# Kernel tuning notes

Measured on AMD Instinct MI355X. Metric: run time of the kernel, lower is better.

## Reference

```python
import jax, jax.numpy as jnp
import numpy as np

D = 256
N_EDGES = 8192
N_CORNERS = 4096


def setup_inputs() -> dict:
    key = jax.random.key(0)
    ks = jax.random.split(key, 8)
    scale = 1.0 / np.sqrt(D)
    return {
        "edge_pred": jax.random.uniform(ks[0], (N_EDGES,), dtype=jnp.float32),
        "edge_corner": jax.random.randint(ks[1], (N_EDGES, 2), 0, N_CORNERS, dtype=jnp.int64),
        "all_corners": jax.random.uniform(ks[2], (N_CORNERS, 2), dtype=jnp.float32),
        "edge_x": jax.random.normal(ks[3], (N_EDGES, D), dtype=jnp.float32),
        "image_x": jax.random.normal(ks[4], (1024,), dtype=jnp.float32),
        "W1": jax.random.normal(ks[5], (D, D), dtype=jnp.float32) * scale,
        "b1": jnp.zeros((D,), dtype=jnp.float32),
        "W2": jax.random.normal(ks[6], (D, D), dtype=jnp.float32) * scale,
        "b2": jnp.zeros((D,), dtype=jnp.float32),
        "W3": jax.random.normal(ks[7], (3 * D, D), dtype=jnp.float32) * scale,
        "b3": jnp.zeros((D,), dtype=jnp.float32),
    }


def _linear_block(x, W, b):
    # LinearBlock: Linear followed by ReLU
    return jax.nn.relu(x @ W + b)


def reference(edge_pred, edge_corner, all_corners, edge_x, image_x, W1, b1, W2, b2, W3, b3):
    # 'fully' branch of MPModule.forward. edge_pred/edge_corner/all_corners/image_x
    # are unused in this branch (kept for signature fidelity).
    e1 = _linear_block(edge_x, W1, b1)              # [N, D]
    # (e1.unsqueeze(1) * e1).mean(-1) == (e1 @ e1.T) / D   -> [N, N]
    sim1 = (e1 @ e1.T) / D
    e2 = _linear_block(edge_x, W2, b2)
    sim2 = (e2 @ e2.T) / D
    # (edge_x * sim.unsqueeze(-1)).sum(1) == sim @ edge_x  -> [N, D]
    agg1 = sim1 @ edge_x
    agg2 = sim2 @ edge_x
    cat = jnp.concatenate([edge_x, agg1, agg2], axis=-1)  # [N, 3D]
    out = _linear_block(cat, W3, b3)                      # [N, D]
    return out
```

## Files before the change

### kernel.cpp

```cpp
#include <hip/hip_runtime.h>

#define NE 8192
#define DD 256
#define NSPLIT 16

typedef __attribute__((ext_vector_type(8))) short short8;
typedef __attribute__((ext_vector_type(4))) short short4v;
typedef __attribute__((ext_vector_type(8))) __bf16 bf16x8;
typedef __attribute__((ext_vector_type(4))) float floatx4;

__device__ __forceinline__ unsigned short f2bf(float f) {
  union { float f; unsigned int i; } v; v.f = f;
  unsigned int r = v.i + 0x7fffu + ((v.i >> 16) & 1u);
  return (unsigned short)(r >> 16);
}

__device__ __forceinline__ floatx4 mfma_bf16(short8 a, short8 b, floatx4 c) {
  return __builtin_amdgcn_mfma_f32_16x16x32_bf16(
      __builtin_bit_cast(bf16x8, a), __builtin_bit_cast(bf16x8, b), c, 0, 0, 0);
}

__device__ __forceinline__ void tcvt_tile(float* ls,
                                          const float* __restrict__ src, int C,
                                          unsigned short* __restrict__ dst, int R,
                                          int r0, int c0, int tid) {
  const int rr = tid >> 4, c4 = (tid & 15) * 4;
#pragma unroll
  for (int k = 0; k < 4; ++k)
    *(floatx4*)&ls[(rr + k * 16) * 68 + c4] =
        *(const floatx4*)&src[(size_t)(r0 + rr + k * 16) * C + c0 + c4];
  __syncthreads();
  const int cc = tid >> 2, rb = (tid & 3) * 16;
  short8 o0, o1;
#pragma unroll
  for (int i = 0; i < 8; ++i) {
    o0[i] = (short)f2bf(ls[(rb + i) * 68 + cc]);
    o1[i] = (short)f2bf(ls[(rb + 8 + i) * 68 + cc]);
  }
  unsigned short* dp = &dst[(size_t)(c0 + cc) * R + r0 + rb];
  *(short8*)dp = o0;
  *(short8*)(dp + 8) = o1;
}

__global__ void cvt_all(const float* __restrict__ x, unsigned short* __restrict__ xb,
                        unsigned short* __restrict__ xT,
                        const float* __restrict__ W1, unsigned short* __restrict__ W1t,
                        const float* __restrict__ W2, unsigned short* __restrict__ W2t,
                        const float* __restrict__ W3, unsigned short* __restrict__ W3t0) {
  __shared__ float ls[64 * 68];
  const int b = blockIdx.x, tid = threadIdx.x;
  if (b < 512) {
    const int p = b & 7, k = b >> 3;
    const int r0 = (16 * p + (k >> 2)) * 64, c0 = (k & 3) * 64;
    const int rr = tid >> 4, c4 = (tid & 15) * 4;
#pragma unroll
    for (int kk = 0; kk < 4; ++kk) {
      floatx4 v = *(const floatx4*)&x[(size_t)(r0 + rr + kk * 16) * DD + c0 + c4];
      *(floatx4*)&ls[(rr + kk * 16) * 68 + c4] = v;
      short4v s;
#pragma unroll
      for (int c = 0; c < 4; ++c) s[c] = (short)f2bf(v[c]);
      *(short4v*)&xb[(size_t)(r0 + rr + kk * 16) * DD + c0 + c4] = s;
    }
    __syncthreads();
    const int cc = tid >> 2, rb = (tid & 3) * 16;
    short8 o0, o1;
#pragma unroll
    for (int i = 0; i < 8; ++i) {
      o0[i] = (short)f2bf(ls[(rb + i) * 68 + cc]);
      o1[i] = (short)f2bf(ls[(rb + 8 + i) * 68 + cc]);
    }
    unsigned short* dp = &xT[(size_t)(c0 + cc) * NE + r0 + rb];
    *(short8*)dp = o0;
    *(short8*)(dp + 8) = o1;
  } else {
    int t = b - 512;
    const float* src = (t < 16) ? W1 : ((t < 32) ? W2 : W3);
    unsigned short* dst = (t < 16) ? W1t : ((t < 32) ? W2t : W3t0);
    t &= 15;
    tcvt_tile(ls, src, DD, dst, DD, (t >> 2) * 64, (t & 3) * 64, tid);
  }
}

__global__ __launch_bounds__(256, 3)
void e_gemm(const unsigned short* __restrict__ xb,
            const unsigned short* __restrict__ W1t, const float* __restrict__ b1,
            const unsigned short* __restrict__ W2t, const float* __restrict__ b2,
            unsigned short* __restrict__ e1, unsigned short* __restrict__ e2,
            unsigned short* __restrict__ e1T, unsigned short* __restrict__ e2T)
{
  __shared__ __align__(16) unsigned short smA[64 * 136];
  __shared__ __align__(16) unsigned short smB1[64 * 136];
  __shared__ __align__(16) unsigned short smB2[64 * 136];
  const int T = threadIdx.x, lane = T & 63, wv = T >> 6;
  const int q = lane >> 4, r = lane & 15;
  const int L = blockIdx.x;
  const int p = L & 7, k = L >> 3;
  const int col0 = (k & 3) * 64, row0 = (16 * p + (k >> 2)) * 64;

  floatx4 acc1[4], acc2[4];
#pragma unroll
  for (int j = 0; j < 4; ++j) {
    acc1[j] = (floatx4){0.f, 0.f, 0.f, 0.f};
    acc2[j] = (floatx4){0.f, 0.f, 0.f, 0.f};
  }

  short8 pa[4], pb1[4], pb2[4];
#pragma unroll
  for (int pp = 0; pp < 4; ++pp) {
    const int id = pp * 256 + T, rr = id >> 4, k8 = (id & 15) * 8;
    pa[pp]  = *(const short8*)&xb[(size_t)(row0 + rr) * DD + k8];
    pb1[pp] = *(const short8*)&W1t[(size_t)(col0 + rr) * DD + k8];
    pb2[pp] = *(const short8*)&W2t[(size_t)(col0 + rr) * DD + k8];
  }

  for (int kc = 0; kc < 256; kc += 128) {
#pragma unroll
    for (int pp = 0; pp < 4; ++pp) {
      const int id = pp * 256 + T, rr = id >> 4, k8 = (id & 15) * 8;
      *(short8*)&smA[rr * 136 + k8]  = pa[pp];
      *(short8*)&smB1[rr * 136 + k8] = pb1[pp];
      *(short8*)&smB2[rr * 136 + k8] = pb2[pp];
    }
    __syncthreads();
    if (kc + 128 < 256) {
#pragma unroll
      for (int pp = 0; pp < 4; ++pp) {
        const int id = pp * 256 + T, rr = id >> 4, k8 = (id & 15) * 8;
        pa[pp]  = *(const short8*)&xb[(size_t)(row0 + rr) * DD + kc + 128 + k8];
        pb1[pp] = *(const short8*)&W1t[(size_t)(col0 + rr) * DD + kc + 128 + k8];
        pb2[pp] = *(const short8*)&W2t[(size_t)(col0 + rr) * DD + kc + 128 + k8];
      }
    }
#pragma unroll
    for (int ks = 0; ks < 4; ++ks) {
      short8 af = *(const short8*)&smA[(wv * 16 + r) * 136 + ks * 32 + q * 8];
#pragma unroll
      for (int j = 0; j < 4; ++j) {
        short8 b1f = *(const short8*)&smB1[(j * 16 + r) * 136 + ks * 32 + q * 8];
        short8 b2f = *(const short8*)&smB2[(j * 16 + r) * 136 + ks * 32 + q * 8];
        acc1[j] = mfma_bf16(af, b1f, acc1[j]);
        acc2[j] = mfma_bf16(af, b2f, acc2[j]);
      }
    }
    __syncthreads();
  }

  unsigned short* t1s = smB1;
  unsigned short* t2s = smB2;
#pragma unroll
  for (int j = 0; j < 4; ++j) {
    const int col = col0 + j * 16 + r;
    const int lc = j * 16 + r;
    const int lr = wv * 16 + q * 4;
    const int rowb = row0 + lr;
    const float b1v = b1[col], b2v = b2[col];
#pragma unroll
    for (int t = 0; t < 4; ++t) {
      unsigned short h1 = f2bf(fmaxf(acc1[j][t] + b1v, 0.0f));
      unsigned short h2 = f2bf(fmaxf(acc2[j][t] + b2v, 0.0f));
      t1s[lc * 68 + lr + t] = h1;
      t2s[lc * 68 + lr + t] = h2;
      e1[(size_t)(rowb + t) * DD + col] = h1;
      e2[(size_t)(rowb + t) * DD + col] = h2;
    }
  }
  __syncthreads();
  {
    const int c = T >> 2, seg = (T & 3) * 16;
    short8 v1a = *(short8*)&t1s[c * 68 + seg];
    short8 v1b = *(short8*)&t1s[c * 68 + seg + 8];
    short8 v2a = *(short8*)&t2s[c * 68 + seg];
    short8 v2b = *(short8*)&t2s[c * 68 + seg + 8];
    unsigned short* d1 = &e1T[(size_t)(col0 + c) * NE + row0 + seg];
    unsigned short* d2 = &e2T[(size_t)(col0 + c) * NE + row0 + seg];
    *(short8*)d1 = v1a; *(short8*)(d1 + 8) = v1b;
    *(short8*)d2 = v2a; *(short8*)(d2 + 8) = v2b;
  }
}

__global__ __launch_bounds__(256, 4)
void atb(const unsigned short* __restrict__ e1T, const unsigned short* __restrict__ e2T,
         const unsigned short* __restrict__ xT, float* __restrict__ P_T)
{
  __shared__ __align__(16) unsigned short smA[64 * 136];
  __shared__ __align__(16) unsigned short smB[64 * 136];
  const int T = threadIdx.x, lane = T & 63, wv = T >> 6;
  const int q = lane >> 4, r = lane & 15;
  const int L = blockIdx.x;
  const int p = L & 7, k = L >> 3;
  const int y = 2 * p + (k & 1);
  const int t2 = k >> 1;
  const int mn = t2 & 15, z = t2 >> 4;
  const int m0 = (mn >> 2) * 64, n0 = (mn & 3) * 64;
  const int j0 = y * (NE / NSPLIT);
  const unsigned short* E = z ? e2T : e1T;
  float* P = P_T + (size_t)(z * NSPLIT + y) * 65536;

  floatx4 acc[4];
#pragma unroll
  for (int j = 0; j < 4; ++j) acc[j] = (floatx4){0.f, 0.f, 0.f, 0.f};

  short8 pa[4], pb[4];
#pragma unroll
  for (int pp = 0; pp < 4; ++pp) {
    const int id = pp * 256 + T, mm = id >> 4, j8 = (id & 15) * 8;
    pa[pp] = *(const short8*)&E[(size_t)(m0 + mm) * NE + j0 + j8];
    pb[pp] = *(const short8*)&xT[(size_t)(n0 + mm) * NE + j0 + j8];
  }

  for (int jc = 0; jc < NE / NSPLIT; jc += 128) {
#pragma unroll
    for (int pp = 0; pp < 4; ++pp) {
      const int id = pp * 256 + T, mm = id >> 4, j8 = (id & 15) * 8;
      *(short8*)&smA[mm * 136 + j8] = pa[pp];
      *(short8*)&smB[mm * 136 + j8] = pb[pp];
    }
    __syncthreads();
    if (jc + 128 < NE / NSPLIT) {
#pragma unroll
      for (int pp = 0; pp < 4; ++pp) {
        const int id = pp * 256 + T, mm = id >> 4, j8 = (id & 15) * 8;
        pa[pp] = *(const short8*)&E[(size_t)(m0 + mm) * NE + j0 + jc + 128 + j8];
        pb[pp] = *(const short8*)&xT[(size_t)(n0 + mm) * NE + j0 + jc + 128 + j8];
      }
    }
#pragma unroll
    for (int ks = 0; ks < 4; ++ks) {
      short8 af = *(const short8*)&smA[(wv * 16 + r) * 136 + ks * 32 + q * 8];
#pragma unroll
      for (int j = 0; j < 4; ++j) {
        short8 bf = *(const short8*)&smB[(j * 16 + r) * 136 + ks * 32 + q * 8];
        acc[j] = mfma_bf16(af, bf, acc[j]);
      }
    }
    __syncthreads();
  }
#pragma unroll
  for (int j = 0; j < 4; ++j) {
    const int n = n0 + j * 16 + r;
    const int m = m0 + wv * 16 + q * 4;
    *(floatx4*)&P[(size_t)n * DD + m] = acc[j];
  }
}

__global__ void reduce_g(const float* __restrict__ P_T, float* __restrict__ G_T) {
  int idx = blockIdx.x * 256 + threadIdx.x;
  int z = idx >> 14, off = idx & 16383;
  const floatx4* Pp = (const floatx4*)P_T;
  floatx4 s = (floatx4){0.f, 0.f, 0.f, 0.f};
#pragma unroll
  for (int y = 0; y < NSPLIT; ++y)
    s += Pp[(size_t)(z * NSPLIT + y) * 16384 + off];
  ((floatx4*)G_T)[idx] = s;
}

__global__ __launch_bounds__(256, 2)
void h_mfma(const float* __restrict__ G_T, const float* __restrict__ W3,
            unsigned short* __restrict__ H1t, unsigned short* __restrict__ H2t)
{
  __shared__ __align__(16) unsigned short smA[64 * 136];
  __shared__ __align__(16) unsigned short smB[64 * 136];
  const int T = threadIdx.x, lane = T & 63, wv = T >> 6;
  const int q = lane >> 4, r = lane & 15;
  const int z = blockIdx.z;
  const int me0 = (blockIdx.x >> 2) * 64, m30 = (blockIdx.x & 3) * 64;
  const float* G = G_T + (size_t)z * 65536;
  unsigned short* Ht = z ? H2t : H1t;
  const int woff = 256 + z * 256;

  floatx4 acc[4];
#pragma unroll
  for (int j = 0; j < 4; ++j) acc[j] = (floatx4){0.f, 0.f, 0.f, 0.f};

  for (int lc = 0; lc < 256; lc += 128) {
#pragma unroll
    for (int pp = 0; pp < 2; ++pp) {
      const int id = pp * 256 + T, lb = id >> 4, e4 = id & 15;
      floatx4 grow[4], wrow[4];
#pragma unroll
      for (int i = 0; i < 4; ++i) {
        grow[i] = *(const floatx4*)&G[(size_t)(lc + lb * 4 + i) * DD + me0 + e4 * 4];
        wrow[i] = *(const floatx4*)&W3[(size_t)(woff + lc + lb * 4 + i) * DD + m30 + e4 * 4];
      }
#pragma unroll
      for (int s4 = 0; s4 < 4; ++s4) {
        const int c = (s4 + e4) & 3;
        short4v ga = {(short)f2bf(grow[0][c] * 0.00390625f),
                      (short)f2bf(grow[1][c] * 0.00390625f),
                      (short)f2bf(grow[2][c] * 0.00390625f),
                      (short)f2bf(grow[3][c] * 0.00390625f)};
        short4v wa = {(short)f2bf(wrow[0][c]), (short)f2bf(wrow[1][c]),
                      (short)f2bf(wrow[2][c]), (short)f2bf(wrow[3][c])};
        *(short4v*)&smA[(e4 * 4 + c) * 136 + lb * 4] = ga;
        *(short4v*)&smB[(e4 * 4 + c) * 136 + lb * 4] = wa;
      }
    }
    __syncthreads();
#pragma unroll
    for (int ks = 0; ks < 4; ++ks) {
      short8 af = *(const short8*)&smA[(wv * 16 + r) * 136 + ks * 32 + q * 8];
#pragma unroll
      for (int j = 0; j < 4; ++j) {
        short8 bf = *(const short8*)&smB[(j * 16 + r) * 136 + ks * 32 + q * 8];
        acc[j] = mfma_bf16(af, bf, acc[j]);
      }
    }
    __syncthreads();
  }
#pragma unroll
  for (int j = 0; j < 4; ++j) {
    const int m3 = m30 + j * 16 + r;
    const int me = me0 + wv * 16 + q * 4;
    short4v v;
#pragma unroll
    for (int i = 0; i < 4; ++i) v[i] = (short)f2bf(acc[j][i]);
    *(short4v*)&Ht[(size_t)m3 * DD + me] = v;
  }
}

__global__ __launch_bounds__(256, 4)
void out_gemm(const unsigned short* __restrict__ xb,
              const unsigned short* __restrict__ e1, const unsigned short* __restrict__ e2,
              const unsigned short* __restrict__ W3t0,
              const unsigned short* __restrict__ H1t, const unsigned short* __restrict__ H2t,
              const float* __restrict__ b3, float* __restrict__ out)
{
  __shared__ __align__(16) unsigned short smA[64 * 136];
  __shared__ __align__(16) unsigned short smB[64 * 136];
  const int T = threadIdx.x, lane = T & 63, wv = T >> 6;
  const int q = lane >> 4, r = lane & 15;
  const int L = blockIdx.x;
  const int p = L & 7, k = L >> 3;
  const int col0 = (k & 3) * 64, row0 = (16 * p + (k >> 2)) * 64;

  const unsigned short* As[3] = {xb, e1, e2};
  const unsigned short* Bs[3] = {W3t0, H1t, H2t};

  floatx4 acc[4];
#pragma unroll
  for (int j = 0; j < 4; ++j) acc[j] = (floatx4){0.f, 0.f, 0.f, 0.f};

  short8 qa[4], qb[4];
#pragma unroll
  for (int pp = 0; pp < 4; ++pp) {
    const int id = pp * 256 + T, rr = id >> 4, k8 = (id & 15) * 8;
    qa[pp] = *(const short8*)&As[0][(size_t)(row0 + rr) * DD + k8];
    qb[pp] = *(const short8*)&Bs[0][(size_t)(col0 + rr) * DD + k8];
  }

  for (int rd = 0; rd < 6; ++rd) {
#pragma unroll
    for (int pp = 0; pp < 4; ++pp) {
      const int id = pp * 256 + T, rr = id >> 4, k8 = (id & 15) * 8;
      *(short8*)&smA[rr * 136 + k8] = qa[pp];
      *(short8*)&smB[rr * 136 + k8] = qb[pp];
    }
    __syncthreads();
    if (rd + 1 < 6) {
      const int s = (rd + 1) >> 1, kc = ((rd + 1) & 1) * 128;
      const unsigned short* A = As[s];
      const unsigned short* B = Bs[s];
#pragma unroll
      for (int pp = 0; pp < 4; ++pp) {
        const int id = pp * 256 + T, rr = id >> 4, k8 = (id & 15) * 8;
        qa[pp] = *(const short8*)&A[(size_t)(row0 + rr) * DD + kc + k8];
        qb[pp] = *(const short8*)&B[(size_t)(col0 + rr) * DD + kc + k8];
      }
    }
#pragma unroll
    for (int ks = 0; ks < 4; ++ks) {
      short8 af = *(const short8*)&smA[(wv * 16 + r) * 136 + ks * 32 + q * 8];
#pragma unroll
      for (int j = 0; j < 4; ++j) {
        short8 bf = *(const short8*)&smB[(j * 16 + r) * 136 + ks * 32 + q * 8];
        acc[j] = mfma_bf16(af, bf, acc[j]);
      }
    }
    __syncthreads();
  }
#pragma unroll
  for (int j = 0; j < 4; ++j) {
    const int col = col0 + j * 16 + r;
    const float bv = b3[col];
    const int rowb = row0 + wv * 16 + q * 4;
#pragma unroll
    for (int t = 0; t < 4; ++t)
      out[(size_t)(rowb + t) * DD + col] = fmaxf(acc[j][t] + bv, 0.0f);
  }
}

extern "C" void kernel_launch(void* const* d_in, const int* in_sizes, int n_in,
                              void* d_out, int out_size, void* d_ws, size_t ws_size,
                              hipStream_t stream) {
  (void)in_sizes; (void)n_in; (void)out_size; (void)ws_size;
  const float* x  = (const float*)d_in[3];
  const float* W1 = (const float*)d_in[5];
  const float* b1 = (const float*)d_in[6];
  const float* W2 = (const float*)d_in[7];
  const float* b2 = (const float*)d_in[8];
  const float* W3 = (const float*)d_in[9];
  const float* b3 = (const float*)d_in[10];
  float* out = (float*)d_out;

  char* ws = (char*)d_ws;
  const size_t MB = 1u << 20;
  const size_t KB = 1u << 10;
  unsigned short* xb   = (unsigned short*)ws;
  unsigned short* xT   = (unsigned short*)(ws + 4 * MB);
  unsigned short* e1   = (unsigned short*)(ws + 8 * MB);
  unsigned short* e2   = (unsigned short*)(ws + 12 * MB);
  unsigned short* e1T  = (unsigned short*)(ws + 16 * MB);
  unsigned short* e2T  = (unsigned short*)(ws + 20 * MB);
  unsigned short* W1t  = (unsigned short*)(ws + 24 * MB);
  unsigned short* W2t  = (unsigned short*)(ws + 24 * MB + 128 * KB);
  unsigned short* W3t0 = (unsigned short*)(ws + 24 * MB + 256 * KB);
  unsigned short* H1t  = (unsigned short*)(ws + 24 * MB + 384 * KB);
  unsigned short* H2t  = (unsigned short*)(ws + 24 * MB + 512 * KB);
  float* G_T           = (float*)(ws + 24 * MB + 640 * KB);
  float* P_T           = (float*)(ws + 25 * MB);

  cvt_all<<<560, 256, 0, stream>>>(x, xb, xT, W1, W1t, W2, W2t, W3, W3t0);
  e_gemm<<<512, 256, 0, stream>>>(xb, W1t, b1, W2t, b2, e1, e2, e1T, e2T);
  atb<<<512, 256, 0, stream>>>(e1T, e2T, xT, P_T);
  reduce_g<<<128, 256, 0, stream>>>(P_T, G_T);
  h_mfma<<<dim3(16, 1, 2), 256, 0, stream>>>(G_T, W3, H1t, H2t);
  out_gemm<<<512, 256, 0, stream>>>(xb, e1, e2, W3t0, H1t, H2t, b3, out);
}
```

Before: 120.4 us.

## Fuse all six stages into one persistent kernel with grid barriers

Replaces the six separate launches (convert, e-GEMM, A^T·B partials, reduction, H GEMM, output GEMM) with one persistent kernel of 256 blocks. Each block handles two tiles per stage, and stages are separated by an atomic-counter grid barrier. The aim is to remove inter-kernel launch gaps and tail drain between the small stages. The partial-sum buffer is aliased onto the output buffer, and a memset resets the barrier counter on every call. In exchange, each CU runs only one 4-wave block instead of several resident blocks, so there is less latency hiding. Correctness also depends on all 256 blocks being co-resident.

```diff
diff --git a/kernel.cpp b/kernel.cpp
--- a/kernel.cpp
+++ b/kernel.cpp
@@ -3,6 +3,7 @@
 #define NE 8192
 #define DD 256
 #define NSPLIT 16
+#define NBLK 256
 
 typedef __attribute__((ext_vector_type(8))) short short8;
 typedef __attribute__((ext_vector_type(4))) short short4v;
@@ -18,6 +19,18 @@
 __device__ __forceinline__ floatx4 mfma_bf16(short8 a, short8 b, floatx4 c) {
   return __builtin_amdgcn_mfma_f32_16x16x32_bf16(
       __builtin_bit_cast(bf16x8, a), __builtin_bit_cast(bf16x8, b), c, 0, 0, 0);
+}
+
+__device__ __forceinline__ void gbar(unsigned* bar, unsigned target) {
+  __syncthreads();
+  if (threadIdx.x == 0) {
+    __threadfence();
+    __hip_atomic_fetch_add(bar, 1u, __ATOMIC_ACQ_REL, __HIP_MEMORY_SCOPE_AGENT);
+    while (__hip_atomic_load(bar, __ATOMIC_ACQUIRE, __HIP_MEMORY_SCOPE_AGENT) < target)
+      __builtin_amdgcn_s_sleep(1);
+    __threadfence();
+  }
+  __syncthreads();
 }
 
 __device__ __forceinline__ void tcvt_tile(float* ls,
@@ -42,351 +55,348 @@
   *(short8*)(dp + 8) = o1;
 }
 
-__global__ void cvt_all(const float* __restrict__ x, unsigned short* __restrict__ xb,
-                        unsigned short* __restrict__ xT,
-                        const float* __restrict__ W1, unsigned short* __restrict__ W1t,
-                        const float* __restrict__ W2, unsigned short* __restrict__ W2t,
-                        const float* __restrict__ W3, unsigned short* __restrict__ W3t0) {
-  __shared__ float ls[64 * 68];
-  const int b = blockIdx.x, tid = threadIdx.x;
-  if (b < 512) {
-    const int p = b & 7, k = b >> 3;
-    const int r0 = (16 * p + (k >> 2)) * 64, c0 = (k & 3) * 64;
-    const int rr = tid >> 4, c4 = (tid & 15) * 4;
-#pragma unroll
-    for (int kk = 0; kk < 4; ++kk) {
-      floatx4 v = *(const floatx4*)&x[(size_t)(r0 + rr + kk * 16) * DD + c0 + c4];
-      *(floatx4*)&ls[(rr + kk * 16) * 68 + c4] = v;
-      short4v s;
-#pragma unroll
-      for (int c = 0; c < 4; ++c) s[c] = (short)f2bf(v[c]);
-      *(short4v*)&xb[(size_t)(r0 + rr + kk * 16) * DD + c0 + c4] = s;
-    }
-    __syncthreads();
-    const int cc = tid >> 2, rb = (tid & 3) * 16;
-    short8 o0, o1;
-#pragma unroll
-    for (int i = 0; i < 8; ++i) {
-      o0[i] = (short)f2bf(ls[(rb + i) * 68 + cc]);
-      o1[i] = (short)f2bf(ls[(rb + 8 + i) * 68 + cc]);
-    }
-    unsigned short* dp = &xT[(size_t)(c0 + cc) * NE + r0 + rb];
-    *(short8*)dp = o0;
-    *(short8*)(dp + 8) = o1;
-  } else {
-    int t = b - 512;
-    const float* src = (t < 16) ? W1 : ((t < 32) ? W2 : W3);
-    unsigned short* dst = (t < 16) ? W1t : ((t < 32) ? W2t : W3t0);
-    t &= 15;
-    tcvt_tile(ls, src, DD, dst, DD, (t >> 2) * 64, (t & 3) * 64, tid);
-  }
-}
-
-__global__ __launch_bounds__(256, 3)
-void e_gemm(const unsigned short* __restrict__ xb,
-            const unsigned short* __restrict__ W1t, const float* __restrict__ b1,
-            const unsigned short* __restrict__ W2t, const float* __restrict__ b2,
-            unsigned short* __restrict__ e1, unsigned short* __restrict__ e2,
-            unsigned short* __restrict__ e1T, unsigned short* __restrict__ e2T)
+__global__ __launch_bounds__(256, 2)
+void mega(const float* __restrict__ x,
+          const float* __restrict__ W1, const float* __restrict__ b1,
+          const float* __restrict__ W2, const float* __restrict__ b2,
+          const float* __restrict__ W3, const float* __restrict__ b3,
+          float* __restrict__ out,
+          unsigned short* __restrict__ xb, unsigned short* __restrict__ xT,
+          unsigned short* __restrict__ e1, unsigned short* __restrict__ e2,
+          unsigned short* __restrict__ e1T, unsigned short* __restrict__ e2T,
+          unsigned short* __restrict__ W1t, unsigned short* __restrict__ W2t,
+          unsigned short* __restrict__ W3t0,
+          unsigned short* __restrict__ H1t, unsigned short* __restrict__ H2t,
+          float* __restrict__ G_T, float* __restrict__ P_T,
+          unsigned* bar)
 {
-  __shared__ __align__(16) unsigned short smA[64 * 136];
-  __shared__ __align__(16) unsigned short smB1[64 * 136];
-  __shared__ __align__(16) unsigned short smB2[64 * 136];
-  const int T = threadIdx.x, lane = T & 63, wv = T >> 6;
+  __shared__ __align__(16) unsigned short smPool[3 * 64 * 136];
+  unsigned short* smA  = smPool;
+  unsigned short* smB1 = smPool + 64 * 136;
+  unsigned short* smB2 = smPool + 2 * 64 * 136;
+  const int b = blockIdx.x, T = threadIdx.x;
+  const int lane = T & 63, wv = T >> 6;
   const int q = lane >> 4, r = lane & 15;
-  const int L = blockIdx.x;
-  const int p = L & 7, k = L >> 3;
-  const int col0 = (k & 3) * 64, row0 = (16 * p + (k >> 2)) * 64;
-
-  floatx4 acc1[4], acc2[4];
-#pragma unroll
-  for (int j = 0; j < 4; ++j) {
-    acc1[j] = (floatx4){0.f, 0.f, 0.f, 0.f};
-    acc2[j] = (floatx4){0.f, 0.f, 0.f, 0.f};
-  }
-
-  short8 pa[4], pb1[4], pb2[4];
-#pragma unroll
-  for (int pp = 0; pp < 4; ++pp) {
-    const int id = pp * 256 + T, rr = id >> 4, k8 = (id & 15) * 8;
-    pa[pp]  = *(const short8*)&xb[(size_t)(row0 + rr) * DD + k8];
-    pb1[pp] = *(const short8*)&W1t[(size_t)(col0 + rr) * DD + k8];
-    pb2[pp] = *(const short8*)&W2t[(size_t)(col0 + rr) * DD + k8];
-  }
-
-  for (int kc = 0; kc < 256; kc += 128) {
+
+  {
+    float* ls = (float*)smPool;
+#pragma unroll
+    for (int h = 0; h < 2; ++h) {
+      const int L = b + h * NBLK;
+      const int p = L & 7, k = L >> 3;
+      const int r0 = (16 * p + (k >> 2)) * 64, c0 = (k & 3) * 64;
+      const int rr = T >> 4, c4 = (T & 15) * 4;
+#pragma unroll
+      for (int kk = 0; kk < 4; ++kk) {
+        floatx4 v = *(const floatx4*)&x[(size_t)(r0 + rr + kk * 16) * DD + c0 + c4];
+        *(floatx4*)&ls[(rr + kk * 16) * 68 + c4] = v;
+        short4v s;
+#pragma unroll
+        for (int c = 0; c < 4; ++c) s[c] = (short)f2bf(v[c]);
+        *(short4v*)&xb[(size_t)(r0 + rr + kk * 16) * DD + c0 + c4] = s;
+      }
+      __syncthreads();
+      const int cc = T >> 2, rb = (T & 3) * 16;
+      short8 o0, o1;
+#pragma unroll
+      for (int i = 0; i < 8; ++i) {
+        o0[i] = (short)f2bf(ls[(rb + i) * 68 + cc]);
+        o1[i] = (short)f2bf(ls[(rb + 8 + i) * 68 + cc]);
+      }
+      unsigned short* dp = &xT[(size_t)(c0 + cc) * NE + r0 + rb];
+      *(short8*)dp = o0;
+      *(short8*)(dp + 8) = o1;
+      __syncthreads();
+    }
+    if (b < 48) {
+      int t = b;
+      const float* src = (t < 16) ? W1 : ((t < 32) ? W2 : W3);
+      unsigned short* dst = (t < 16) ? W1t : ((t < 32) ? W2t : W3t0);
+      t &= 15;
+      tcvt_tile(ls, src, DD, dst, DD, (t >> 2) * 64, (t & 3) * 64, T);
+    }
+  }
+  gbar(bar, 1 * NBLK);
+
+#pragma unroll 1
+  for (int h = 0; h < 2; ++h) {
+    const int L = b + h * NBLK;
+    const int p = L & 7, k = L >> 3;
+    const int col0 = (k & 3) * 64, row0 = (16 * p + (k >> 2)) * 64;
+
+    floatx4 acc1[4], acc2[4];
+#pragma unroll
+    for (int j = 0; j < 4; ++j) {
+      acc1[j] = (floatx4){0.f, 0.f, 0.f, 0.f};
+      acc2[j] = (floatx4){0.f, 0.f, 0.f, 0.f};
+    }
+
+    short8 pa[4], pb1[4], pb2[4];
 #pragma unroll
     for (int pp = 0; pp < 4; ++pp) {
       const int id = pp * 256 + T, rr = id >> 4, k8 = (id & 15) * 8;
-      *(short8*)&smA[rr * 136 + k8]  = pa[pp];
-      *(short8*)&smB1[rr * 136 + k8] = pb1[pp];
-      *(short8*)&smB2[rr * 136 + k8] = pb2[pp];
-    }
-    __syncthreads();
-    if (kc + 128 < 256) {
+      pa[pp]  = *(const short8*)&xb[(size_t)(row0 + rr) * DD + k8];
+      pb1[pp] = *(const short8*)&W1t[(size_t)(col0 + rr) * DD + k8];
+      pb2[pp] = *(const short8*)&W2t[(size_t)(col0 + rr) * DD + k8];
+    }
+
+    for (int kc = 0; kc < 256; kc += 128) {
 #pragma unroll
       for (int pp = 0; pp < 4; ++pp) {
         const int id = pp * 256 + T, rr = id >> 4, k8 = (id & 15) * 8;
-        pa[pp]  = *(const short8*)&xb[(size_t)(row0 + rr) * DD + kc + 128 + k8];
-        pb1[pp] = *(const short8*)&W1t[(size_t)(col0 + rr) * DD + kc + 128 + k8];
-        pb2[pp] = *(const short8*)&W2t[(size_t)(col0 + rr) * DD + kc + 128 + k8];
-      }
-    }
-#pragma unroll
-    for (int ks = 0; ks < 4; ++ks) {
-      short8 af = *(const short8*)&smA[(wv * 16 + r) * 136 + ks * 32 + q * 8];
-#pragma unroll
-      for (int j = 0; j < 4; ++j) {
-        short8 b1f = *(const short8*)&smB1[(j * 16 + r) * 136 + ks * 32 + q * 8];
-        short8 b2f = *(const short8*)&smB2[(j * 16 + r) * 136 + ks * 32 + q * 8];
-        acc1[j] = mfma_bf16(af, b1f, acc1[j]);
-        acc2[j] = mfma_bf16(af, b2f, acc2[j]);
+        *(short8*)&smA[rr * 136 + k8]  = pa[pp];
+        *(short8*)&smB1[rr * 136 + k8] = pb1[pp];
+        *(short8*)&smB2[rr * 136 + k8] = pb2[pp];
+      }
+      __syncthreads();
+      if (kc + 128 < 256) {
+#pragma unroll
+        for (int pp = 0; pp < 4; ++pp) {
+          const int id = pp * 256 + T, rr = id >> 4, k8 = (id & 15) * 8;
+          pa[pp]  = *(const short8*)&xb[(size_t)(row0 + rr) * DD + kc + 128 + k8];
+          pb1[pp] = *(const short8*)&W1t[(size_t)(col0 + rr) * DD + kc + 128 + k8];
+          pb2[pp] = *(const short8*)&W2t[(size_t)(col0 + rr) * DD + kc + 128 + k8];
+        }
+      }
+#pragma unroll
+      for (int ks = 0; ks < 4; ++ks) {
+        short8 af = *(const short8*)&smA[(wv * 16 + r) * 136 + ks * 32 + q * 8];
+#pragma unroll
+        for (int j = 0; j < 4; ++j) {
+          short8 b1f = *(const short8*)&smB1[(j * 16 + r) * 136 + ks * 32 + q * 8];
+          short8 b2f = *(const short8*)&smB2[(j * 16 + r) * 136 + ks * 32 + q * 8];
+          acc1[j] = mfma_bf16(af, b1f, acc1[j]);
+          acc2[j] = mfma_bf16(af, b2f, acc2[j]);
+        }
+      }
+      __syncthreads();
+    }
+
+    unsigned short* t1s = smB1;
+    unsigned short* t2s = smB2;
+#pragma unroll
+    for (int j = 0; j < 4; ++j) {
+      const int col = col0 + j * 16 + r;
+      const int lc = j * 16 + r;
+      const int lr = wv * 16 + q * 4;
+      const int rowb = row0 + lr;
+      const float b1v = b1[col], b2v = b2[col];
+#pragma unroll
+      for (int t = 0; t < 4; ++t) {
+        unsigned short h1 = f2bf(fmaxf(acc1[j][t] + b1v, 0.0f));
+        unsigned short h2 = f2bf(fmaxf(acc2[j][t] + b2v, 0.0f));
+        t1s[lc * 68 + lr + t] = h1;
+        t2s[lc * 68 + lr + t] = h2;
+        e1[(size_t)(rowb + t) * DD + col] = h1;
+        e2[(size_t)(rowb + t) * DD + col] = h2;
       }
     }
     __syncthreads();
-  }
-
-  unsigned short* t1s = smB1;
-  unsigned short* t2s = smB2;
-#pragma unroll
-  for (int j = 0; j < 4; ++j) {
-    const int col = col0 + j * 16 + r;
-    const int lc = j * 16 + r;
-    const int lr = wv * 16 + q * 4;
-    const int rowb = row0 + lr;
-    const float b1v = b1[col], b2v = b2[col];
-#pragma unroll
-    for (int t = 0; t < 4; ++t) {
-      unsigned short h1 = f2bf(fmaxf(acc1[j][t] + b1v, 0.0f));
-      unsigned short h2 = f2bf(fmaxf(acc2[j][t] + b2v, 0.0f));
-      t1s[lc * 68 + lr + t] = h1;
-      t2s[lc * 68 + lr + t] = h2;
-      e1[(size_t)(rowb + t) * DD + col] = h1;
-      e2[(size_t)(rowb + t) * DD + col] = h2;
-    }
-  }
-  __syncthreads();
-  {
-    const int c = T >> 2, seg = (T & 3) * 16;
-    short8 v1a = *(short8*)&t1s[c * 68 + seg];
-    short8 v1b = *(short8*)&t1s[c * 68 + seg + 8];
-    short8 v2a = *(short8*)&t2s[c * 68 + seg];
-    short8 v2b = *(short8*)&t2s[c * 68 + seg + 8];
-    unsigned short* d1 = &e1T[(size_t)(col0 + c) * NE + row0 + seg];
-    unsigned short* d2 = &e2T[(size_t)(col0 + c) * NE + row0 + seg];
-    *(short8*)d1 = v1a; *(short8*)(d1 + 8) = v1b;
-    *(short8*)d2 = v2a; *(short8*)(d2 + 8) = v2b;
-  }
-}
-
-__global__ __launch_bounds__(256, 4)
-void atb(const unsigned short* __restrict__ e1T, const unsigned short* __restrict__ e2T,
-         const unsigned short* __restrict__ xT, float* __restrict__ P_T)
-{
-  __shared__ __align__(16) unsigned short smA[64 * 136];
-  __shared__ __align__(16) unsigned short smB[64 * 136];
-  const int T = threadIdx.x, lane = T & 63, wv = T >> 6;
-  const int q = lane >> 4, r = lane & 15;
-  const int L = blockIdx.x;
-  const int p = L & 7, k = L >> 3;
-  const int y = 2 * p + (k & 1);
-  const int t2 = k >> 1;
-  const int mn = t2 & 15, z = t2 >> 4;
-  const int m0 = (mn >> 2) * 64, n0 = (mn & 3) * 64;
-  const int j0 = y * (NE / NSPLIT);
-  const unsigned short* E = z ? e2T : e1T;
-  float* P = P_T + (size_t)(z * NSPLIT + y) * 65536;
-
-  floatx4 acc[4];
-#pragma unroll
-  for (int j = 0; j < 4; ++j) acc[j] = (floatx4){0.f, 0.f, 0.f, 0.f};
-
-  short8 pa[4], pb[4];
-#pragma unroll
-  for (int pp = 0; pp < 4; ++pp) {
-    const int id = pp * 256 + T, mm = id >> 4, j8 = (id & 15) * 8;
-    pa[pp] = *(const short8*)&E[(size_t)(m0 + mm) * NE + j0 + j8];
-    pb[pp] = *(const short8*)&xT[(size_t)(n0 + mm) * NE + j0 + j8];
-  }
-
-  for (int jc = 0; jc < NE / NSPLIT; jc += 128) {
+    {
+      const int c = T >> 2, seg = (T & 3) * 16;
+      short8 v1a = *(short8*)&t1s[c * 68 + seg];
+      short8 v1b = *(short8*)&t1s[c * 68 + seg + 8];
+      short8 v2a = *(short8*)&t2s[c * 68 + seg];
+      short8 v2b = *(short8*)&t2s[c * 68 + seg + 8];
+      unsigned short* d1 = &e1T[(size_t)(col0 + c) * NE + row0 + seg];
+      unsigned short* d2 = &e2T[(size_t)(col0 + c) * NE + row0 + seg];
+      *(short8*)d1 = v1a; *(short8*)(d1 + 8) = v1b;
+      *(short8*)d2 = v2a; *(short8*)(d2 + 8) = v2b;
+    }
+    __syncthreads();
+  }
+  gbar(bar, 2 * NBLK);
+
+#pragma unroll 1
+  for (int h = 0; h < 2; ++h) {
+    const int L = b + h * NBLK;
+    const int p = L & 7, k = L >> 3;
+    const int y = 2 * p + (k & 1);
+    const int t2 = k >> 1;
+    const int mn = t2 & 15, z = t2 >> 4;
+    const int m0 = (mn >> 2) * 64, n0 = (mn & 3) * 64;
+    const int j0 = y * (NE / NSPLIT);
+    const unsigned short* E = z ? e2T : e1T;
+    float* P = P_T + (size_t)(z * NSPLIT + y) * 65536;
+
+    floatx4 acc[4];
+#pragma unroll
+    for (int j = 0; j < 4; ++j) acc[j] = (floatx4){0.f, 0.f, 0.f, 0.f};
+
+    short8 pa[4], pb[4];
 #pragma unroll
     for (int pp = 0; pp < 4; ++pp) {
       const int id = pp * 256 + T, mm = id >> 4, j8 = (id & 15) * 8;
-      *(short8*)&smA[mm * 136 + j8] = pa[pp];
-      *(short8*)&smB[mm * 136 + j8] = pb[pp];
-    }
-    __syncthreads();
-    if (jc + 128 < NE / NSPLIT) {
+      pa[pp] = *(const short8*)&E[(size_t)(m0 + mm) * NE + j0 + j8];
+      pb[pp] = *(const short8*)&xT[(size_t)(n0 + mm) * NE + j0 + j8];
+    }
+
+    for (int jc = 0; jc < NE / NSPLIT; jc += 128) {
 #pragma unroll
       for (int pp = 0; pp < 4; ++pp) {
         const int id = pp * 256 + T, mm = id >> 4, j8 = (id & 15) * 8;
-        pa[pp] = *(const short8*)&E[(size_t)(m0 + mm) * NE + j0 + jc + 128 + j8];
-        pb[pp] = *(const short8*)&xT[(size_t)(n0 + mm) * NE + j0 + jc + 128 + j8];
-      }
-    }
-#pragma unroll
-    for (int ks = 0; ks < 4; ++ks) {
-      short8 af = *(const short8*)&smA[(wv * 16 + r) * 136 + ks * 32 + q * 8];
-#pragma unroll
-      for (int j = 0; j < 4; ++j) {
-        short8 bf = *(const short8*)&smB[(j * 16 + r) * 136 + ks * 32 + q * 8];
-        acc[j] = mfma_bf16(af, bf, acc[j]);
-      }
-    }
-    __syncthreads();
-  }
-#pragma unroll
-  for (int j = 0; j < 4; ++j) {
-    const int n = n0 + j * 16 + r;
-    const int m = m0 + wv * 16 + q * 4;
-    *(floatx4*)&P[(size_t)n * DD + m] = acc[j];
-  }
-}
-
-__global__ void reduce_g(const float* __restrict__ P_T, float* __restrict__ G_T) {
-  int idx = blockIdx.x * 256 + threadIdx.x;
-  int z = idx >> 14, off = idx & 16383;
-  const floatx4* Pp = (const floatx4*)P_T;
-  floatx4 s = (floatx4){0.f, 0.f, 0.f, 0.f};
-#pragma unroll
-  for (int y = 0; y < NSPLIT; ++y)
-    s += Pp[(size_t)(z * NSPLIT + y) * 16384 + off];
-  ((floatx4*)G_T)[idx] = s;
-}
-
-__global__ __launch_bounds__(256, 2)
-void h_mfma(const float* __restrict__ G_T, const float* __restrict__ W3,
-            unsigned short* __restrict__ H1t, unsigned short* __restrict__ H2t)
-{
-  __shared__ __align__(16) unsigned short smA[64 * 136];
-  __shared__ __align__(16) unsigned short smB[64 * 136];
-  const int T = threadIdx.x, lane = T & 63, wv = T >> 6;
-  const int q = lane >> 4, r = lane & 15;
-  const int z = blockIdx.z;
-  const int me0 = (blockIdx.x >> 2) * 64, m30 = (blockIdx.x & 3) * 64;
-  const float* G = G_T + (size_t)z * 65536;
-  unsigned short* Ht = z ? H2t : H1t;
-  const int woff = 256 + z * 256;
-
-  floatx4 acc[4];
-#pragma unroll
-  for (int j = 0; j < 4; ++j) acc[j] = (floatx4){0.f, 0.f, 0.f, 0.f};
-
-  for (int lc = 0; lc < 256; lc += 128) {
-#pragma unroll
-    for (int pp = 0; pp < 2; ++pp) {
-      const int id = pp * 256 + T, lb = id >> 4, e4 = id & 15;
-      floatx4 grow[4], wrow[4];
-#pragma unroll
-      for (int i = 0; i < 4; ++i) {
-        grow[i] = *(const floatx4*)&G[(size_t)(lc + lb * 4 + i) * DD + me0 + e4 * 4];
-        wrow[i] = *(const floatx4*)&W3[(size_t)(woff + lc + lb * 4 + i) * DD + m30 + e4 * 4];
-      }
-#pragma unroll
-      for (int s4 = 0; s4 < 4; ++s4) {
-        const int c = (s4 + e4) & 3;
-        short4v ga = {(short)f2bf(grow[0][c] * 0.00390625f),
-                      (short)f2bf(grow[1][c] * 0.00390625f),
-                      (short)f2bf(grow[2][c] * 0.00390625f),
-                      (short)f2bf(grow[3][c] * 0.00390625f)};
-        short4v wa = {(short)f2bf(wrow[0][c]), (short)f2bf(wrow[1][c]),
-                      (short)f2bf(wrow[2][c]), (short)f2bf(wrow[3][c])};
-        *(short4v*)&smA[(e4 * 4 + c) * 136 + lb * 4] = ga;
-        *(short4v*)&smB[(e4 * 4 + c) * 136 + lb * 4] = wa;
-      }
-    }
-    __syncthreads();
-#pragma unroll
-    for (int ks = 0; ks < 4; ++ks) {
-      short8 af = *(const short8*)&smA[(wv * 16 + r) * 136 + ks * 32 + q * 8];
-#pragma unroll
-      for (int j = 0; j < 4; ++j) {
-        short8 bf = *(const short8*)&smB[(j * 16 + r) * 136 + ks * 32 + q * 8];
-        acc[j] = mfma_bf16(af, bf, acc[j]);
-      }
-    }
-    __syncthreads();
-  }
-#pragma unroll
-  for (int j = 0; j < 4; ++j) {
-    const int m3 = m30 + j * 16 + r;
-    const int me = me0 + wv * 16 + q * 4;
-    short4v v;
-#pragma unroll
-    for (int i = 0; i < 4; ++i) v[i] = (short)f2bf(acc[j][i]);
-    *(short4v*)&Ht[(size_t)m3 * DD + me] = v;
-  }
-}
-
-__global__ __launch_bounds__(256, 4)
-void out_gemm(const unsigned short* __restrict__ xb,
-              const unsigned short* __restrict__ e1, const unsigned short* __restrict__ e2,
-              const unsigned short* __restrict__ W3t0,
-              const unsigned short* __restrict__ H1t, const unsigned short* __restrict__ H2t,
-              const float* __restrict__ b3, float* __restrict__ out)
-{
-  __shared__ __align__(16) unsigned short smA[64 * 136];
-  __shared__ __align__(16) unsigned short smB[64 * 136];
-  const int T = threadIdx.x, lane = T & 63, wv = T >> 6;
-  const int q = lane >> 4, r = lane & 15;
-  const int L = blockIdx.x;
-  const int p = L & 7, k = L >> 3;
-  const int col0 = (k & 3) * 64, row0 = (16 * p + (k >> 2)) * 64;
-
-  const unsigned short* As[3] = {xb, e1, e2};
-  const unsigned short* Bs[3] = {W3t0, H1t, H2t};
-
-  floatx4 acc[4];
-#pragma unroll
-  for (int j = 0; j < 4; ++j) acc[j] = (floatx4){0.f, 0.f, 0.f, 0.f};
-
-  short8 qa[4], qb[4];
-#pragma unroll
-  for (int pp = 0; pp < 4; ++pp) {
-    const int id = pp * 256 + T, rr = id >> 4, k8 = (id & 15) * 8;
-    qa[pp] = *(const short8*)&As[0][(size_t)(row0 + rr) * DD + k8];
-    qb[pp] = *(const short8*)&Bs[0][(size_t)(col0 + rr) * DD + k8];
-  }
-
-  for (int rd = 0; rd < 6; ++rd) {
+        *(short8*)&smA[mm * 136 + j8] = pa[pp];
+        *(short8*)&smB1[mm * 136 + j8] = pb[pp];
+      }
+      __syncthreads();
+      if (jc + 128 < NE / NSPLIT) {
+#pragma unroll
+        for (int pp = 0; pp < 4; ++pp) {
+          const int id = pp * 256 + T, mm = id >> 4, j8 = (id & 15) * 8;
+          pa[pp] = *(const short8*)&E[(size_t)(m0 + mm) * NE + j0 + jc + 128 + j8];
+          pb[pp] = *(const short8*)&xT[(size_t)(n0 + mm) * NE + j0 + jc + 128 + j8];
+        }
+      }
+#pragma unroll
+      for (int ks = 0; ks < 4; ++ks) {
+        short8 af = *(const short8*)&smA[(wv * 16 + r) * 136 + ks * 32 + q * 8];
+#pragma unroll
+        for (int j = 0; j < 4; ++j) {
+          short8 bf = *(const short8*)&smB1[(j * 16 + r) * 136 + ks * 32 + q * 8];
+          acc[j] = mfma_bf16(af, bf, acc[j]);
+        }
+      }
+      __syncthreads();
+    }
+#pragma unroll
+    for (int j = 0; j < 4; ++j) {
+      const int n = n0 + j * 16 + r;
+      const int m = m0 + wv * 16 + q * 4;
+      *(floatx4*)&P[(size_t)n * DD + m] = acc[j];
+    }
+  }
+  gbar(bar, 3 * NBLK);
+
+  if (b < 128) {
+    int idx = b * 256 + T;
+    int z = idx >> 14, off = idx & 16383;
+    const floatx4* Pp = (const floatx4*)P_T;
+    floatx4 s = (floatx4){0.f, 0.f, 0.f, 0.f};
+#pragma unroll
+    for (int y = 0; y < NSPLIT; ++y)
+      s += Pp[(size_t)(z * NSPLIT + y) * 16384 + off];
+    ((floatx4*)G_T)[idx] = s;
+  }
+  gbar(bar, 4 * NBLK);
+
+  if (b < 32) {
+    const int z = b >> 4, bx = b & 15;
+    const int me0 = (bx >> 2) * 64, m30 = (bx & 3) * 64;
+    const float* G = G_T + (size_t)z * 65536;
+    unsigned short* Ht = z ? H2t : H1t;
+    const int woff = 256 + z * 256;
+
+    floatx4 acc[4];
+#pragma unroll
+    for (int j = 0; j < 4; ++j) acc[j] = (floatx4){0.f, 0.f, 0.f, 0.f};
+
+    for (int lc = 0; lc < 256; lc += 128) {
+#pragma unroll
+      for (int pp = 0; pp < 2; ++pp) {
+        const int id = pp * 256 + T, lb = id >> 4, e4 = id & 15;
+        floatx4 grow[4], wrow[4];
+#pragma unroll
+        for (int i = 0; i < 4; ++i) {
+          grow[i] = *(const floatx4*)&G[(size_t)(lc + lb * 4 + i) * DD + me0 + e4 * 4];
+          wrow[i] = *(const floatx4*)&W3[(size_t)(woff + lc + lb * 4 + i) * DD + m30 + e4 * 4];
+        }
+#pragma unroll
+        for (int s4 = 0; s4 < 4; ++s4) {
+          const int c = (s4 + e4) & 3;
+          short4v ga = {(short)f2bf(grow[0][c] * 0.00390625f),
+                        (short)f2bf(grow[1][c] * 0.00390625f),
+                        (short)f2bf(grow[2][c] * 0.00390625f),
+                        (short)f2bf(grow[3][c] * 0.00390625f)};
+          short4v wa = {(short)f2bf(wrow[0][c]), (short)f2bf(wrow[1][c]),
+                        (short)f2bf(wrow[2][c]), (short)f2bf(wrow[3][c])};
+          *(short4v*)&smA[(e4 * 4 + c) * 136 + lb * 4] = ga;
+          *(short4v*)&smB1[(e4 * 4 + c) * 136 + lb * 4] = wa;
+        }
+      }
+      __syncthreads();
+#pragma unroll
+      for (int ks = 0; ks < 4; ++ks) {
+        short8 af = *(const short8*)&smA[(wv * 16 + r) * 136 + ks * 32 + q * 8];
+#pragma unroll
+        for (int j = 0; j < 4; ++j) {
+          short8 bf = *(const short8*)&smB1[(j * 16 + r) * 136 + ks * 32 + q * 8];
+          acc[j] = mfma_bf16(af, bf, acc[j]);
+        }
+      }
+      __syncthreads();
+    }
+#pragma unroll
+    for (int j = 0; j < 4; ++j) {
+      const int m3 = m30 + j * 16 + r;
+      const int me = me0 + wv * 16 + q * 4;
+      short4v v;
+#pragma unroll
+      for (int i = 0; i < 4; ++i) v[i] = (short)f2bf(acc[j][i]);
+      *(short4v*)&Ht[(size_t)m3 * DD + me] = v;
+    }
+  }
+  gbar(bar, 5 * NBLK);
+
+#pragma unroll 1
+  for (int h = 0; h < 2; ++h) {
+    const int L = b + h * NBLK;
+    const int p = L & 7, k = L >> 3;
+    const int col0 = (k & 3) * 64, row0 = (16 * p + (k >> 2)) * 64;
+
+    const unsigned short* As[3] = {xb, e1, e2};
+    const unsigned short* Bs[3] = {W3t0, H1t, H2t};
+
+    floatx4 acc[4];
+#pragma unroll
+    for (int j = 0; j < 4; ++j) acc[j] = (floatx4){0.f, 0.f, 0.f, 0.f};
+
+    short8 qa[4], qb[4];
 #pragma unroll
     for (int pp = 0; pp < 4; ++pp) {
       const int id = pp * 256 + T, rr = id >> 4, k8 = (id & 15) * 8;
-      *(short8*)&smA[rr * 136 + k8] = qa[pp];
-      *(short8*)&smB[rr * 136 + k8] = qb[pp];
-    }
-    __syncthreads();
-    if (rd + 1 < 6) {
-      const int s = (rd + 1) >> 1, kc = ((rd + 1) & 1) * 128;
-      const unsigned short* A = As[s];
-      const unsigned short* B = Bs[s];
+      qa[pp] = *(const short8*)&As[0][(size_t)(row0 + rr) * DD + k8];
+      qb[pp] = *(const short8*)&Bs[0][(size_t)(col0 + rr) * DD + k8];
+    }
+
+    for (int rd = 0; rd < 6; ++rd) {
 #pragma unroll
       for (int pp = 0; pp < 4; ++pp) {
         const int id = pp * 256 + T, rr = id >> 4, k8 = (id & 15) * 8;
-        qa[pp] = *(const short8*)&A[(size_t)(row0 + rr) * DD + kc + k8];
-        qb[pp] = *(const short8*)&B[(size_t)(col0 + rr) * DD + kc + k8];
-      }
-    }
-#pragma unroll
-    for (int ks = 0; ks < 4; ++ks) {
-      short8 af = *(const short8*)&smA[(wv * 16 + r) * 136 + ks * 32 + q * 8];
-#pragma unroll
-      for (int j = 0; j < 4; ++j) {
-        short8 bf = *(const short8*)&smB[(j * 16 + r) * 136 + ks * 32 + q * 8];
-        acc[j] = mfma_bf16(af, bf, acc[j]);
-      }
-    }
-    __syncthreads();
-  }
-#pragma unroll
-  for (int j = 0; j < 4; ++j) {
-    const int col = col0 + j * 16 + r;
-    const float bv = b3[col];
-    const int rowb = row0 + wv * 16 + q * 4;
-#pragma unroll
-    for (int t = 0; t < 4; ++t)
-      out[(size_t)(rowb + t) * DD + col] = fmaxf(acc[j][t] + bv, 0.0f);
+        *(short8*)&smA[rr * 136 + k8] = qa[pp];
+        *(short8*)&smB1[rr * 136 + k8] = qb[pp];
+      }
+      __syncthreads();
+      if (rd + 1 < 6) {
+        const int s = (rd + 1) >> 1, kc = ((rd + 1) & 1) * 128;
+        const unsigned short* A = As[s];
+        const unsigned short* B = Bs[s];
+#pragma unroll
+        for (int pp = 0; pp < 4; ++pp) {
+          const int id = pp * 256 + T, rr = id >> 4, k8 = (id & 15) * 8;
+          qa[pp] = *(const short8*)&A[(size_t)(row0 + rr) * DD + kc + k8];
+          qb[pp] = *(const short8*)&B[(size_t)(col0 + rr) * DD + kc + k8];
+        }
+      }
+#pragma unroll
+      for (int ks = 0; ks < 4; ++ks) {
+        short8 af = *(const short8*)&smA[(wv * 16 + r) * 136 + ks * 32 + q * 8];
+#pragma unroll
+        for (int j = 0; j < 4; ++j) {
+          short8 bf = *(const short8*)&smB1[(j * 16 + r) * 136 + ks * 32 + q * 8];
+          acc[j] = mfma_bf16(af, bf, acc[j]);
+        }
+      }
+      __syncthreads();
+    }
+#pragma unroll
+    for (int j = 0; j < 4; ++j) {
+      const int col = col0 + j * 16 + r;
+      const float bv = b3[col];
+      const int rowb = row0 + wv * 16 + q * 4;
+#pragma unroll
+      for (int t = 0; t < 4; ++t)
+        out[(size_t)(rowb + t) * DD + col] = fmaxf(acc[j][t] + bv, 0.0f);
+    }
   }
 }
 
@@ -418,12 +428,12 @@
   unsigned short* H1t  = (unsigned short*)(ws + 24 * MB + 384 * KB);
   unsigned short* H2t  = (unsigned short*)(ws + 24 * MB + 512 * KB);
   float* G_T           = (float*)(ws + 24 * MB + 640 * KB);
-  float* P_T           = (float*)(ws + 25 * MB);
-
-  cvt_all<<<560, 256, 0, stream>>>(x, xb, xT, W1, W1t, W2, W2t, W3, W3t0);
-  e_gemm<<<512, 256, 0, stream>>>(xb, W1t, b1, W2t, b2, e1, e2, e1T, e2T);
-  atb<<<512, 256, 0, stream>>>(e1T, e2T, xT, P_T);
-  reduce_g<<<128, 256, 0, stream>>>(P_T, G_T);
-  h_mfma<<<dim3(16, 1, 2), 256, 0, stream>>>(G_T, W3, H1t, H2t);
-  out_gemm<<<512, 256, 0, stream>>>(xb, e1, e2, W3t0, H1t, H2t, b3, out);
-}
+  unsigned* bar        = (unsigned*)(ws + 24 * MB + 1152 * KB);
+  float* P_T           = (float*)d_out;
+
+  hipMemsetAsync(bar, 0, 128, stream);
+
+  mega<<<NBLK, 256, 0, stream>>>(x, W1, b1, W2, b2, W3, b3, out,
+                                 xb, xT, e1, e2, e1T, e2T, W1t, W2t, W3t0,
+                                 H1t, H2t, G_T, P_T, bar);
+}
```

New measurement: 278.9 us. 2.32x slower.

## Fuse e1/e2 partial Gram products sharing x tile, store bf16 partials

Applied to the files above, without the earlier changes.

The atb kernel now computes both e1^T x and e2^T x in one block, so each x tile loaded into shared memory is reused for two accumulators. The split-K factor doubles to keep the grid at 512 blocks. Partial sums are written as bf16 instead of fp32 and summed in fp32 by reduce_g, which halves partial-buffer traffic. The cost is more registers and LDS per block (occupancy hint lowered to 3) and extra rounding error from bf16 partials across 32 splits.

```diff
diff --git a/kernel.cpp b/kernel.cpp
--- a/kernel.cpp
+++ b/kernel.cpp
@@ -2,7 +2,7 @@
 
 #define NE 8192
 #define DD 256
-#define NSPLIT 16
+#define NSPLIT 32
 
 typedef __attribute__((ext_vector_type(8))) short short8;
 typedef __attribute__((ext_vector_type(4))) short short4v;
@@ -13,6 +13,11 @@
   union { float f; unsigned int i; } v; v.f = f;
   unsigned int r = v.i + 0x7fffu + ((v.i >> 16) & 1u);
   return (unsigned short)(r >> 16);
+}
+
+__device__ __forceinline__ float bf2f(unsigned short h) {
+  union { unsigned int i; float f; } v; v.i = ((unsigned int)h) << 16;
+  return v.f;
 }
 
 __device__ __forceinline__ floatx4 mfma_bf16(short8 a, short8 b, floatx4 c) {
@@ -179,80 +184,96 @@
   }
 }
 
-__global__ __launch_bounds__(256, 4)
+__global__ __launch_bounds__(256, 3)
 void atb(const unsigned short* __restrict__ e1T, const unsigned short* __restrict__ e2T,
-         const unsigned short* __restrict__ xT, float* __restrict__ P_T)
+         const unsigned short* __restrict__ xT, unsigned short* __restrict__ P_T)
 {
-  __shared__ __align__(16) unsigned short smA[64 * 136];
-  __shared__ __align__(16) unsigned short smB[64 * 136];
+  __shared__ __align__(16) unsigned short smE1[64 * 136];
+  __shared__ __align__(16) unsigned short smE2[64 * 136];
+  __shared__ __align__(16) unsigned short smX[64 * 136];
   const int T = threadIdx.x, lane = T & 63, wv = T >> 6;
   const int q = lane >> 4, r = lane & 15;
   const int L = blockIdx.x;
   const int p = L & 7, k = L >> 3;
-  const int y = 2 * p + (k & 1);
-  const int t2 = k >> 1;
-  const int mn = t2 & 15, z = t2 >> 4;
+  const int mn = k >> 2;
+  const int y = 4 * p + (k & 3);
   const int m0 = (mn >> 2) * 64, n0 = (mn & 3) * 64;
   const int j0 = y * (NE / NSPLIT);
-  const unsigned short* E = z ? e2T : e1T;
-  float* P = P_T + (size_t)(z * NSPLIT + y) * 65536;
-
-  floatx4 acc[4];
-#pragma unroll
-  for (int j = 0; j < 4; ++j) acc[j] = (floatx4){0.f, 0.f, 0.f, 0.f};
-
-  short8 pa[4], pb[4];
+
+  floatx4 acc1[4], acc2[4];
+#pragma unroll
+  for (int j = 0; j < 4; ++j) {
+    acc1[j] = (floatx4){0.f, 0.f, 0.f, 0.f};
+    acc2[j] = (floatx4){0.f, 0.f, 0.f, 0.f};
+  }
+
+  short8 pe1[4], pe2[4], px[4];
 #pragma unroll
   for (int pp = 0; pp < 4; ++pp) {
     const int id = pp * 256 + T, mm = id >> 4, j8 = (id & 15) * 8;
-    pa[pp] = *(const short8*)&E[(size_t)(m0 + mm) * NE + j0 + j8];
-    pb[pp] = *(const short8*)&xT[(size_t)(n0 + mm) * NE + j0 + j8];
+    pe1[pp] = *(const short8*)&e1T[(size_t)(m0 + mm) * NE + j0 + j8];
+    pe2[pp] = *(const short8*)&e2T[(size_t)(m0 + mm) * NE + j0 + j8];
+    px[pp]  = *(const short8*)&xT[(size_t)(n0 + mm) * NE + j0 + j8];
   }
 
   for (int jc = 0; jc < NE / NSPLIT; jc += 128) {
 #pragma unroll
     for (int pp = 0; pp < 4; ++pp) {
       const int id = pp * 256 + T, mm = id >> 4, j8 = (id & 15) * 8;
-      *(short8*)&smA[mm * 136 + j8] = pa[pp];
-      *(short8*)&smB[mm * 136 + j8] = pb[pp];
+      *(short8*)&smE1[mm * 136 + j8] = pe1[pp];
+      *(short8*)&smE2[mm * 136 + j8] = pe2[pp];
+      *(short8*)&smX[mm * 136 + j8]  = px[pp];
     }
     __syncthreads();
     if (jc + 128 < NE / NSPLIT) {
 #pragma unroll
       for (int pp = 0; pp < 4; ++pp) {
         const int id = pp * 256 + T, mm = id >> 4, j8 = (id & 15) * 8;
-        pa[pp] = *(const short8*)&E[(size_t)(m0 + mm) * NE + j0 + jc + 128 + j8];
-        pb[pp] = *(const short8*)&xT[(size_t)(n0 + mm) * NE + j0 + jc + 128 + j8];
+        pe1[pp] = *(const short8*)&e1T[(size_t)(m0 + mm) * NE + j0 + jc + 128 + j8];
+        pe2[pp] = *(const short8*)&e2T[(size_t)(m0 + mm) * NE + j0 + jc + 128 + j8];
+        px[pp]  = *(const short8*)&xT[(size_t)(n0 + mm) * NE + j0 + jc + 128 + j8];
       }
     }
 #pragma unroll
     for (int ks = 0; ks < 4; ++ks) {
-      short8 af = *(const short8*)&smA[(wv * 16 + r) * 136 + ks * 32 + q * 8];
+      short8 a1 = *(const short8*)&smE1[(wv * 16 + r) * 136 + ks * 32 + q * 8];
+      short8 a2 = *(const short8*)&smE2[(wv * 16 + r) * 136 + ks * 32 + q * 8];
 #pragma unroll
       for (int j = 0; j < 4; ++j) {
-        short8 bf = *(const short8*)&smB[(j * 16 + r) * 136 + ks * 32 + q * 8];
-        acc[j] = mfma_bf16(af, bf, acc[j]);
-      }
-    }
-    __syncthreads();
-  }
+        short8 bx = *(const short8*)&smX[(j * 16 + r) * 136 + ks * 32 + q * 8];
+        acc1[j] = mfma_bf16(a1, bx, acc1[j]);
+        acc2[j] = mfma_bf16(a2, bx, acc2[j]);
+      }
+    }
+    __syncthreads();
+  }
+
 #pragma unroll
   for (int j = 0; j < 4; ++j) {
     const int n = n0 + j * 16 + r;
     const int m = m0 + wv * 16 + q * 4;
-    *(floatx4*)&P[(size_t)n * DD + m] = acc[j];
-  }
-}
-
-__global__ void reduce_g(const float* __restrict__ P_T, float* __restrict__ G_T) {
+    short4v s1, s2;
+#pragma unroll
+    for (int t = 0; t < 4; ++t) {
+      s1[t] = (short)f2bf(acc1[j][t]);
+      s2[t] = (short)f2bf(acc2[j][t]);
+    }
+    *(short4v*)&P_T[(size_t)y * 65536 + n * DD + m] = s1;
+    *(short4v*)&P_T[(size_t)(NSPLIT + y) * 65536 + n * DD + m] = s2;
+  }
+}
+
+__global__ void reduce_g(const unsigned short* __restrict__ P_T, float* __restrict__ G_T) {
   int idx = blockIdx.x * 256 + threadIdx.x;
-  int z = idx >> 14, off = idx & 16383;
-  const floatx4* Pp = (const floatx4*)P_T;
+  int z = idx >> 14, off = (idx & 16383) * 4;
   floatx4 s = (floatx4){0.f, 0.f, 0.f, 0.f};
 #pragma unroll
-  for (int y = 0; y < NSPLIT; ++y)
-    s += Pp[(size_t)(z * NSPLIT + y) * 16384 + off];
-  ((floatx4*)G_T)[idx] = s;
+  for (int y = 0; y < NSPLIT; ++y) {
+    short4v v = *(const short4v*)&P_T[(size_t)(z * NSPLIT + y) * 65536 + off];
+#pragma unroll
+    for (int c = 0; c < 4; ++c) s[c] += bf2f((unsigned short)v[c]);
+  }
+  *(floatx4*)&G_T[(size_t)z * 65536 + off] = s;
 }
 
 __global__ __launch_bounds__(256, 2)
@@ -418,7 +439,7 @@
   unsigned short* H1t  = (unsigned short*)(ws + 24 * MB + 384 * KB);
   unsigned short* H2t  = (unsigned short*)(ws + 24 * MB + 512 * KB);
   float* G_T           = (float*)(ws + 24 * MB + 640 * KB);
-  float* P_T           = (float*)(ws + 25 * MB);
+  unsigned short* P_T  = (unsigned short*)(ws + 25 * MB);
 
   cvt_all<<<560, 256, 0, stream>>>(x, xb, xT, W1, W1t, W2, W2t, W3, W3t0);
   e_gemm<<<512, 256, 0, stream>>>(xb, W1t, b1, W2t, b2, e1, e2, e1T, e2T);
```

New measurement: 121.7 us. Within noise of the previous version (+1.0%).
